# Performance work log

Hardware: AMD Instinct MI355X
Metric: run time of the kernel (lower is better)

Reference implementation:

```python
import jax, jax.numpy as jnp
import numpy as np

GAMMA0 = 1.0


def patch_to_image(patches):
    # patches: [b, n_patch, patch_dim, 1, T] -> image [b, 1, g*p, g*p, T]
    b, n_patch, patch_dim, _, T = patches.shape
    p = int(patch_dim ** 0.5)
    g = int(n_patch ** 0.5)
    img = patches[:, :, :, 0, :]                      # [b, n_patch, p*p, T]
    img = jnp.transpose(img, (0, 3, 1, 2))            # [b, T, n_patch, p*p]
    img = img.reshape(b, T, g, g, p, p)
    img = jnp.transpose(img, (0, 1, 2, 4, 3, 5)).reshape(b, T, 1, g * p, g * p)
    return jnp.transpose(img, (0, 2, 3, 4, 1))        # [b, 1, g*p, g*p, T]


def setup_inputs() -> dict:
    key = jax.random.key(0)
    k0, k1, k2, k3, k4, k5 = jax.random.split(key, 6)
    X = jax.random.normal(k0, (32, 64, 300, 1, 50), dtype=jnp.float32)
    U = jax.random.normal(k1, (32, 1, 40, 1, 50), dtype=jnp.float32)
    x0 = jax.random.normal(k2, (32, 64, 300, 1), dtype=jnp.float32)
    # dictionaries, column-normalized like torch's norm(dim=2, keepdim=True)
    A = jax.random.uniform(k3, (300, 300), dtype=jnp.float32)
    A = A / jnp.linalg.norm(A, axis=0, keepdims=True)
    B = jax.random.uniform(k4, (300, 40), dtype=jnp.float32)
    B = B / jnp.linalg.norm(B, axis=0, keepdims=True)
    C = jax.random.uniform(k5, (256, 300), dtype=jnp.float32)
    C = C / jnp.linalg.norm(C, axis=0, keepdims=True)
    return {"X": X, "U": U, "x0": x0, "A": A, "B": B, "C": C}


def reference(X, U, x0, A, B, C):
    # X: [b, P, 300, 1, T]  U: [b, 1, 40, 1, T]  x0: [b, P, 300, 1]
    # Prediction x_hat_t = A @ x_{t-1}, with x_{-1} = x0 (vectorized over T)
    x_prev = jnp.concatenate([x0[..., None], X[..., :-1]], axis=-1)   # [b,P,300,1,T]
    X_pred = jnp.einsum('ij,bpjut->bpiut', A, x_prev)                 # [b,P,300,1,T]
    # Reconstruction recon_t = C @ x_t, assembled into frames
    recon = jnp.einsum('dj,bpjut->bpdut', C, X)                       # [b,P,256,1,T]
    vid_recon = patch_to_image(recon)                                 # [b,1,128,128,T]
    # Cause state: gamma_t * sum_patches |x_t|
    Bu = jnp.einsum('ij,bqjut->bqiut', B, U)                          # [b,1,300,1,T]
    gamma = GAMMA0 * (1.0 + jnp.exp(-Bu)) / 2.0
    X_U = gamma * jnp.sum(jnp.abs(X), axis=1, keepdims=True)          # [b,1,300,1,T]
    return (vid_recon, X_pred, X_U)
```

## Files before the change

### kernel.cpp

```cpp
#include <hip/hip_runtime.h>

typedef _Float16 half8 __attribute__((ext_vector_type(8)));
typedef _Float16 half4v __attribute__((ext_vector_type(4)));
typedef float f32x4 __attribute__((ext_vector_type(4)));

#define OFF_PRED 26214400
#define OFF_XU   56934400


__global__ void build_M(const float* __restrict__ A, const float* __restrict__ C,
                        _Float16* __restrict__ M) {
    int idx = blockIdx.x * 256 + threadIdx.x;
    if (idx >= 640 * 320) return;
    int e    = idx & 7;
    int lane = (idx >> 3) & 63;
    int fs   = idx >> 9;
    int mt = fs / 10, ks = fs % 10;
    int m = mt * 16 + (lane & 15);
    int k = ks * 32 + (lane >> 4) * 8 + e;
    float v = 0.f;
    if (k < 300) {
        if (m < 256) v = C[m * 300 + k];
        else if (m < 556) v = A[(m - 256) * 300 + k];
    }
    M[idx] = (_Float16)v;
}

__global__ __launch_bounds__(1024, 1) void gemm_main(
    const float* __restrict__ X, const float* __restrict__ x0,
    const _Float16* __restrict__ M, float* __restrict__ out)
{
    __shared__ _Float16 lds[64 * 320];
    char* ldsb = (char*)lds;
    const int bp = blockIdx.x;
    const int b = bp >> 6, p = bp & 63;
    const int tid = threadIdx.x;
    const float* Xbp = X + bp * 15000;

    const int wave = tid >> 6, lane = tid & 63;
    const int lr = lane & 15, lg = lane >> 4;
    const int g = wave >> 1, h = wave & 1;

    if (tid < 320) {
        int row = tid / 5, c = tid % 5;
        *(half4v*)(ldsb + row * 640 + ((600 + c * 8) ^ ((row & 7) << 4))) =
            (half4v){(_Float16)0.f, (_Float16)0.f, (_Float16)0.f, (_Float16)0.f};
    }
    if (tid < 75) {
        const float* s = x0 + bp * 300 + tid * 4;
        half4v h4 = { (_Float16)s[0], (_Float16)s[1], (_Float16)s[2], (_Float16)s[3] };
        *(half4v*)(ldsb + tid * 8) = h4;
    }
    for (int i = tid; i < 3750; i += 1024) {
        int t = i % 50, jq = i / 50;
        const float* s = Xbp + (jq * 4) * 50 + t;
        half4v h4 = { (_Float16)s[0], (_Float16)s[50], (_Float16)s[100], (_Float16)s[150] };
        int row = t + 1;
        *(half4v*)(ldsb + row * 640 + ((jq * 8) ^ ((row & 7) << 4))) = h4;
    }
    __syncthreads();

    f32x4 acc[5][2];
    #pragma unroll
    for (int j = 0; j < 5; j++)
        #pragma unroll
        for (int nt = 0; nt < 2; nt++)
            acc[j][nt] = (f32x4){0.f, 0.f, 0.f, 0.f};

    const _Float16* Mw = M + (g * 5 * 10) * 512 + lane * 8;
    #define LDSA(nt, ks) (*(const half8*)(ldsb + (h * 32 + (nt) * 16 + lr) * 640 + \
                         (((ks) * 64 + lg * 16) ^ ((lr & 7) << 4))))

    #pragma unroll
    for (int ks = 0; ks < 10; ks++) {
        half8 bf0 = *(const half8*)(Mw + (0 * 10 + ks) * 512);
        half8 bf1 = *(const half8*)(Mw + (1 * 10 + ks) * 512);
        half8 bf2 = *(const half8*)(Mw + (2 * 10 + ks) * 512);
        half8 bf3 = *(const half8*)(Mw + (3 * 10 + ks) * 512);
        half8 bf4 = *(const half8*)(Mw + (4 * 10 + ks) * 512);
        #pragma unroll
        for (int nt = 0; nt < 2; nt++) {
            half8 a = LDSA(nt, ks);
            acc[0][nt] = __builtin_amdgcn_mfma_f32_16x16x32_f16(a, bf0, acc[0][nt], 0, 0, 0);
            acc[1][nt] = __builtin_amdgcn_mfma_f32_16x16x32_f16(a, bf1, acc[1][nt], 0, 0, 0);
            acc[2][nt] = __builtin_amdgcn_mfma_f32_16x16x32_f16(a, bf2, acc[2][nt], 0, 0, 0);
            acc[3][nt] = __builtin_amdgcn_mfma_f32_16x16x32_f16(a, bf3, acc[3][nt], 0, 0, 0);
            acc[4][nt] = __builtin_amdgcn_mfma_f32_16x16x32_f16(a, bf4, acc[4][nt], 0, 0, 0);
        }
    }

    const int gr = p >> 3, gc = p & 7;
    #pragma unroll
    for (int j = 0; j < 5; j++) {
        int colm = g * 80 + j * 16 + lr;
        if (colm < 256) {
            int base = b * 819200 + ((gr * 16 + (colm >> 4)) * 128 + gc * 16 + (colm & 15)) * 50;
            #pragma unroll
            for (int nt = 0; nt < 2; nt++) {
                int t0 = h * 32 + nt * 16 + lg * 4;
                if (t0 == 0) {
                    out[base + 0] = acc[j][0][1];
                    out[base + 1] = acc[j][0][2];
                    out[base + 2] = acc[j][0][3];
                } else if (t0 <= 46) {
                    f32x4 v = acc[j][nt];
                    __builtin_memcpy(&out[base + t0 - 1], &v, 16);
                } else if (t0 == 48) {
                    out[base + 47] = acc[j][nt][0];
                    out[base + 48] = acc[j][nt][1];
                    out[base + 49] = acc[j][nt][2];
                }
            }
        } else if (colm < 556) {
            int base = OFF_PRED + (bp * 300 + (colm - 256)) * 50;
            #pragma unroll
            for (int nt = 0; nt < 2; nt++) {
                int t0 = h * 32 + nt * 16 + lg * 4;
                if (t0 <= 46) {
                    f32x4 v = acc[j][nt];
                    __builtin_memcpy(&out[base + t0], &v, 16);
                } else if (t0 == 48) {
                    out[base + 48] = acc[j][nt][0];
                    out[base + 49] = acc[j][nt][1];
                }
            }
        }
    }
}

__global__ void xu_kernel(const float* __restrict__ X, const float* __restrict__ U,
                          const float* __restrict__ B, float* __restrict__ out) {
    int id = blockIdx.x * 256 + threadIdx.x;
    if (id >= 480000) return;
    int t = id % 50;
    int i = (id / 50) % 300;
    int b = id / 15000;
    const float* xp = X + b * 960000 + i * 50 + t;
    float s = 0.f;
    #pragma unroll 8
    for (int pp = 0; pp < 64; pp++) s += fabsf(xp[pp * 15000]);
    float bu = 0.f;
    const float* up = U + b * 2000 + t;
    const float* Bp = B + i * 40;
    #pragma unroll 8
    for (int q = 0; q < 40; q++) bu += Bp[q] * up[q * 50];
    out[OFF_XU + id] = 0.5f * (1.f + expf(-bu)) * s;
}

extern "C" void kernel_launch(void* const* d_in, const int* in_sizes, int n_in,
                              void* d_out, int out_size, void* d_ws, size_t ws_size,
                              hipStream_t stream) {
    const float* X  = (const float*)d_in[0];
    const float* U  = (const float*)d_in[1];
    const float* x0 = (const float*)d_in[2];
    const float* A  = (const float*)d_in[3];
    const float* B  = (const float*)d_in[4];
    const float* C  = (const float*)d_in[5];
    float* out = (float*)d_out;
    _Float16* M = (_Float16*)d_ws;

    build_M<<<800, 256, 0, stream>>>(A, C, M);
    gemm_main<<<2048, 1024, 0, stream>>>(X, x0, M, out);
    xu_kernel<<<1875, 256, 0, stream>>>(X, U, B, out);
}
```

Baseline: 147.1 us.

## Split each patch GEMM block into two half-time blocks for higher occupancy

```diff
diff --git a/kernel.cpp b/kernel.cpp
--- a/kernel.cpp
+++ b/kernel.cpp
@@ -6,7 +6,6 @@
 
 #define OFF_PRED 26214400
 #define OFF_XU   56934400
-
 
 __global__ void build_M(const float* __restrict__ A, const float* __restrict__ C,
                         _Float16* __restrict__ M) {
@@ -26,37 +25,52 @@
     M[idx] = (_Float16)v;
 }
 
-__global__ __launch_bounds__(1024, 1) void gemm_main(
+#define LDSH(r, j, v) *(_Float16*)(ldsb + (r) * 640 + (((j) * 2) ^ (((r) & 7) << 4))) = (v)
+
+__global__ __launch_bounds__(512, 4) void gemm_main(
     const float* __restrict__ X, const float* __restrict__ x0,
     const _Float16* __restrict__ M, float* __restrict__ out)
 {
-    __shared__ _Float16 lds[64 * 320];
+    __shared__ _Float16 lds[32 * 320];
     char* ldsb = (char*)lds;
-    const int bp = blockIdx.x;
+    const int bid = blockIdx.x;
+    const int bp = bid >> 1, h = bid & 1;
     const int b = bp >> 6, p = bp & 63;
     const int tid = threadIdx.x;
     const float* Xbp = X + bp * 15000;
 
     const int wave = tid >> 6, lane = tid & 63;
     const int lr = lane & 15, lg = lane >> 4;
-    const int g = wave >> 1, h = wave & 1;
+    const int g = wave;
 
-    if (tid < 320) {
-        int row = tid / 5, c = tid % 5;
-        *(half4v*)(ldsb + row * 640 + ((600 + c * 8) ^ ((row & 7) << 4))) =
-            (half4v){(_Float16)0.f, (_Float16)0.f, (_Float16)0.f, (_Float16)0.f};
-    }
-    if (tid < 75) {
-        const float* s = x0 + bp * 300 + tid * 4;
-        half4v h4 = { (_Float16)s[0], (_Float16)s[1], (_Float16)s[2], (_Float16)s[3] };
-        *(half4v*)(ldsb + tid * 8) = h4;
-    }
-    for (int i = tid; i < 3750; i += 1024) {
-        int t = i % 50, jq = i / 50;
-        const float* s = Xbp + (jq * 4) * 50 + t;
-        half4v h4 = { (_Float16)s[0], (_Float16)s[50], (_Float16)s[100], (_Float16)s[150] };
-        int row = t + 1;
-        *(half4v*)(ldsb + row * 640 + ((jq * 8) ^ ((row & 7) << 4))) = h4;
+    #pragma unroll
+    for (int it = 0; it < 5; it++)
+        *(unsigned long long*)(ldsb + tid * 8 + it * 4096) = 0ULL;
+    __syncthreads();
+
+    if (h == 0) {
+        if (tid < 75) {
+            f32x4 v = *(const f32x4*)(x0 + bp * 300 + tid * 4);
+            half4v h4 = { (_Float16)v.x, (_Float16)v.y, (_Float16)v.z, (_Float16)v.w };
+            *(half4v*)(ldsb + tid * 8) = h4;
+        }
+        for (int i = tid; i < 4800; i += 512) {
+            int j = i >> 4, pi = i & 15;
+            int t0 = pi * 2;
+            const float* s = Xbp + j * 50 + t0;
+            float v0 = s[0], v1 = s[1];
+            LDSH(t0 + 1, j, (_Float16)v0);
+            if (pi < 15) LDSH(t0 + 2, j, (_Float16)v1);
+        }
+    } else {
+        for (int i = tid; i < 3000; i += 512) {
+            int j = i / 10, pi = i - (i / 10) * 10;
+            int t0 = 30 + pi * 2;
+            const float* s = Xbp + j * 50 + t0;
+            float v0 = s[0], v1 = s[1];
+            if (pi > 0) LDSH(t0 - 31, j, (_Float16)v0);
+            LDSH(t0 - 30, j, (_Float16)v1);
+        }
     }
     __syncthreads();
 
@@ -67,8 +81,8 @@
         for (int nt = 0; nt < 2; nt++)
             acc[j][nt] = (f32x4){0.f, 0.f, 0.f, 0.f};
 
-    const _Float16* Mw = M + (g * 5 * 10) * 512 + lane * 8;
-    #define LDSA(nt, ks) (*(const half8*)(ldsb + (h * 32 + (nt) * 16 + lr) * 640 + \
+    const _Float16* Mw = M + g * 50 * 512 + lane * 8;
+    #define LDSA(nt, ks) (*(const half8*)(ldsb + ((nt) * 16 + lr) * 640 + \
                          (((ks) * 64 + lg * 16) ^ ((lr & 7) << 4))))
 
     #pragma unroll
@@ -160,6 +174,6 @@
     _Float16* M = (_Float16*)d_ws;
 
     build_M<<<800, 256, 0, stream>>>(A, C, M);
-    gemm_main<<<2048, 1024, 0, stream>>>(X, x0, M, out);
+    gemm_main<<<4096, 512, 0, stream>>>(X, x0, M, out);
     xu_kernel<<<1875, 256, 0, stream>>>(X, U, B, out);
 }
```

Result: slower. 179.6 us (+22.1%).

## Make gemm_main persistent over 8 patches with double-buffered LDS prefetch

Applied to the files above, without the earlier changes.

```diff
diff --git a/kernel.cpp b/kernel.cpp
--- a/kernel.cpp
+++ b/kernel.cpp
@@ -6,7 +6,7 @@
 
 #define OFF_PRED 26214400
 #define OFF_XU   56934400
-
+#define NBP 8
 
 __global__ void build_M(const float* __restrict__ A, const float* __restrict__ C,
                         _Float16* __restrict__ M) {
@@ -30,102 +30,157 @@
     const float* __restrict__ X, const float* __restrict__ x0,
     const _Float16* __restrict__ M, float* __restrict__ out)
 {
-    __shared__ _Float16 lds[64 * 320];
-    char* ldsb = (char*)lds;
-    const int bp = blockIdx.x;
-    const int b = bp >> 6, p = bp & 63;
+    extern __shared__ char ldsraw[];
     const int tid = threadIdx.x;
-    const float* Xbp = X + bp * 15000;
-
     const int wave = tid >> 6, lane = tid & 63;
     const int lr = lane & 15, lg = lane >> 4;
     const int g = wave >> 1, h = wave & 1;
-
-    if (tid < 320) {
-        int row = tid / 5, c = tid % 5;
-        *(half4v*)(ldsb + row * 640 + ((600 + c * 8) ^ ((row & 7) << 4))) =
-            (half4v){(_Float16)0.f, (_Float16)0.f, (_Float16)0.f, (_Float16)0.f};
-    }
-    if (tid < 75) {
-        const float* s = x0 + bp * 300 + tid * 4;
-        half4v h4 = { (_Float16)s[0], (_Float16)s[1], (_Float16)s[2], (_Float16)s[3] };
-        *(half4v*)(ldsb + tid * 8) = h4;
-    }
-    for (int i = tid; i < 3750; i += 1024) {
-        int t = i % 50, jq = i / 50;
-        const float* s = Xbp + (jq * 4) * 50 + t;
-        half4v h4 = { (_Float16)s[0], (_Float16)s[50], (_Float16)s[100], (_Float16)s[150] };
-        int row = t + 1;
-        *(half4v*)(ldsb + row * 640 + ((jq * 8) ^ ((row & 7) << 4))) = h4;
-    }
+    const int bp0 = blockIdx.x * NBP;
+
+    int st_t[4], st_j[4];
+    #pragma unroll
+    for (int u = 0; u < 4; u++) { int i = tid + u * 1024; st_t[u] = i % 50; st_j[u] = i / 50; }
+    const bool v3 = tid < 678;
+
+    const _Float16* Mw = M + g * 50 * 512 + lane * 8;
+
+    #pragma unroll
+    for (int u = 0; u < 10; u++)
+        *(unsigned long long*)(ldsraw + tid * 8 + u * 8192) = 0ULL;
     __syncthreads();
 
-    f32x4 acc[5][2];
-    #pragma unroll
-    for (int j = 0; j < 5; j++)
-        #pragma unroll
-        for (int nt = 0; nt < 2; nt++)
-            acc[j][nt] = (f32x4){0.f, 0.f, 0.f, 0.f};
-
-    const _Float16* Mw = M + (g * 5 * 10) * 512 + lane * 8;
-    #define LDSA(nt, ks) (*(const half8*)(ldsb + (h * 32 + (nt) * 16 + lr) * 640 + \
-                         (((ks) * 64 + lg * 16) ^ ((lr & 7) << 4))))
-
-    #pragma unroll
-    for (int ks = 0; ks < 10; ks++) {
-        half8 bf0 = *(const half8*)(Mw + (0 * 10 + ks) * 512);
-        half8 bf1 = *(const half8*)(Mw + (1 * 10 + ks) * 512);
-        half8 bf2 = *(const half8*)(Mw + (2 * 10 + ks) * 512);
-        half8 bf3 = *(const half8*)(Mw + (3 * 10 + ks) * 512);
-        half8 bf4 = *(const half8*)(Mw + (4 * 10 + ks) * 512);
-        #pragma unroll
-        for (int nt = 0; nt < 2; nt++) {
-            half8 a = LDSA(nt, ks);
-            acc[0][nt] = __builtin_amdgcn_mfma_f32_16x16x32_f16(a, bf0, acc[0][nt], 0, 0, 0);
-            acc[1][nt] = __builtin_amdgcn_mfma_f32_16x16x32_f16(a, bf1, acc[1][nt], 0, 0, 0);
-            acc[2][nt] = __builtin_amdgcn_mfma_f32_16x16x32_f16(a, bf2, acc[2][nt], 0, 0, 0);
-            acc[3][nt] = __builtin_amdgcn_mfma_f32_16x16x32_f16(a, bf3, acc[3][nt], 0, 0, 0);
-            acc[4][nt] = __builtin_amdgcn_mfma_f32_16x16x32_f16(a, bf4, acc[4][nt], 0, 0, 0);
-        }
-    }
-
-    const int gr = p >> 3, gc = p & 7;
-    #pragma unroll
-    for (int j = 0; j < 5; j++) {
-        int colm = g * 80 + j * 16 + lr;
-        if (colm < 256) {
-            int base = b * 819200 + ((gr * 16 + (colm >> 4)) * 128 + gc * 16 + (colm & 15)) * 50;
+    float sx[4][4];
+    float s0x[4];
+
+    {
+        const float* Xb = X + bp0 * 15000;
+        #pragma unroll
+        for (int u = 0; u < 4; u++) if (u < 3 || v3) {
+            const float* s = Xb + st_j[u] * 200 + st_t[u];
+            sx[u][0] = s[0]; sx[u][1] = s[50]; sx[u][2] = s[100]; sx[u][3] = s[150];
+        }
+        if (tid < 75) {
+            f32x4 v = *(const f32x4*)(x0 + bp0 * 300 + tid * 4);
+            s0x[0] = v.x; s0x[1] = v.y; s0x[2] = v.z; s0x[3] = v.w;
+        }
+    }
+    {
+        char* wb = ldsraw;
+        #pragma unroll
+        for (int u = 0; u < 4; u++) if (u < 3 || v3) {
+            int row = st_t[u] + 1;
+            half4v h4 = {(_Float16)sx[u][0], (_Float16)sx[u][1], (_Float16)sx[u][2], (_Float16)sx[u][3]};
+            *(half4v*)(wb + row * 640 + ((st_j[u] * 8) ^ ((row & 7) << 4))) = h4;
+        }
+        if (tid < 75) {
+            half4v h4 = {(_Float16)s0x[0], (_Float16)s0x[1], (_Float16)s0x[2], (_Float16)s0x[3]};
+            *(half4v*)(wb + tid * 8) = h4;
+        }
+    }
+    __syncthreads();
+
+    #define LDSA(base, nt, ks) (*(const half8*)((base) + (h * 32 + (nt) * 16 + lr) * 640 + \
+                               (((ks) * 64 + lg * 16) ^ ((lr & 7) << 4))))
+
+    for (int it = 0; it < NBP; ++it) {
+        const int bp = bp0 + it;
+        const int b = bp >> 6, p = bp & 63;
+        char* ldsb = ldsraw + (it & 1) * 40960;
+
+        if (it + 1 < NBP) {
+            const float* Xb = X + (bp + 1) * 15000;
+            #pragma unroll
+            for (int u = 0; u < 4; u++) if (u < 3 || v3) {
+                const float* s = Xb + st_j[u] * 200 + st_t[u];
+                sx[u][0] = s[0]; sx[u][1] = s[50]; sx[u][2] = s[100]; sx[u][3] = s[150];
+            }
+            if (tid < 75) {
+                f32x4 v = *(const f32x4*)(x0 + (bp + 1) * 300 + tid * 4);
+                s0x[0] = v.x; s0x[1] = v.y; s0x[2] = v.z; s0x[3] = v.w;
+            }
+        }
+
+        f32x4 acc[5][2];
+        #pragma unroll
+        for (int j = 0; j < 5; j++)
+            #pragma unroll
+            for (int nt = 0; nt < 2; nt++)
+                acc[j][nt] = (f32x4){0.f, 0.f, 0.f, 0.f};
+
+        #pragma unroll
+        for (int ks = 0; ks < 10; ks++) {
+            half8 bf0 = *(const half8*)(Mw + (0 * 10 + ks) * 512);
+            half8 bf1 = *(const half8*)(Mw + (1 * 10 + ks) * 512);
+            half8 bf2 = *(const half8*)(Mw + (2 * 10 + ks) * 512);
+            half8 bf3 = *(const half8*)(Mw + (3 * 10 + ks) * 512);
+            half8 bf4 = *(const half8*)(Mw + (4 * 10 + ks) * 512);
             #pragma unroll
             for (int nt = 0; nt < 2; nt++) {
-                int t0 = h * 32 + nt * 16 + lg * 4;
-                if (t0 == 0) {
-                    out[base + 0] = acc[j][0][1];
-                    out[base + 1] = acc[j][0][2];
-                    out[base + 2] = acc[j][0][3];
-                } else if (t0 <= 46) {
-                    f32x4 v = acc[j][nt];
-                    __builtin_memcpy(&out[base + t0 - 1], &v, 16);
-                } else if (t0 == 48) {
-                    out[base + 47] = acc[j][nt][0];
-                    out[base + 48] = acc[j][nt][1];
-                    out[base + 49] = acc[j][nt][2];
+                half8 a = LDSA(ldsb, nt, ks);
+                acc[0][nt] = __builtin_amdgcn_mfma_f32_16x16x32_f16(a, bf0, acc[0][nt], 0, 0, 0);
+                acc[1][nt] = __builtin_amdgcn_mfma_f32_16x16x32_f16(a, bf1, acc[1][nt], 0, 0, 0);
+                acc[2][nt] = __builtin_amdgcn_mfma_f32_16x16x32_f16(a, bf2, acc[2][nt], 0, 0, 0);
+                acc[3][nt] = __builtin_amdgcn_mfma_f32_16x16x32_f16(a, bf3, acc[3][nt], 0, 0, 0);
+                acc[4][nt] = __builtin_amdgcn_mfma_f32_16x16x32_f16(a, bf4, acc[4][nt], 0, 0, 0);
+            }
+        }
+
+        {
+            const int gr = p >> 3, gc = p & 7;
+            #pragma unroll
+            for (int j = 0; j < 5; j++) {
+                int colm = g * 80 + j * 16 + lr;
+                if (colm < 256) {
+                    int base = b * 819200 + ((gr * 16 + (colm >> 4)) * 128 + gc * 16 + (colm & 15)) * 50;
+                    #pragma unroll
+                    for (int nt = 0; nt < 2; nt++) {
+                        int t0 = h * 32 + nt * 16 + lg * 4;
+                        if (t0 == 0) {
+                            out[base + 0] = acc[j][0][1];
+                            out[base + 1] = acc[j][0][2];
+                            out[base + 2] = acc[j][0][3];
+                        } else if (t0 <= 46) {
+                            f32x4 v = acc[j][nt];
+                            __builtin_memcpy(&out[base + t0 - 1], &v, 16);
+                        } else if (t0 == 48) {
+                            out[base + 47] = acc[j][nt][0];
+                            out[base + 48] = acc[j][nt][1];
+                            out[base + 49] = acc[j][nt][2];
+                        }
+                    }
+                } else if (colm < 556) {
+                    int base = OFF_PRED + (bp * 300 + (colm - 256)) * 50;
+                    #pragma unroll
+                    for (int nt = 0; nt < 2; nt++) {
+                        int t0 = h * 32 + nt * 16 + lg * 4;
+                        if (t0 <= 46) {
+                            f32x4 v = acc[j][nt];
+                            __builtin_memcpy(&out[base + t0], &v, 16);
+                        } else if (t0 == 48) {
+                            out[base + 48] = acc[j][nt][0];
+                            out[base + 49] = acc[j][nt][1];
+                        }
+                    }
                 }
             }
-        } else if (colm < 556) {
-            int base = OFF_PRED + (bp * 300 + (colm - 256)) * 50;
-            #pragma unroll
-            for (int nt = 0; nt < 2; nt++) {
-                int t0 = h * 32 + nt * 16 + lg * 4;
-                if (t0 <= 46) {
-                    f32x4 v = acc[j][nt];
-                    __builtin_memcpy(&out[base + t0], &v, 16);
-                } else if (t0 == 48) {
-                    out[base + 48] = acc[j][nt][0];
-                    out[base + 49] = acc[j][nt][1];
-                }
-            }
-        }
-    }
+        }
+
+        if (it + 1 < NBP) {
+            char* wb = ldsraw + ((it & 1) ^ 1) * 40960;
+            #pragma unroll
+            for (int u = 0; u < 4; u++) if (u < 3 || v3) {
+                int row = st_t[u] + 1;
+                half4v h4 = {(_Float16)sx[u][0], (_Float16)sx[u][1], (_Float16)sx[u][2], (_Float16)sx[u][3]};
+                *(half4v*)(wb + row * 640 + ((st_j[u] * 8) ^ ((row & 7) << 4))) = h4;
+            }
+            if (tid < 75) {
+                half4v h4 = {(_Float16)s0x[0], (_Float16)s0x[1], (_Float16)s0x[2], (_Float16)s0x[3]};
+                *(half4v*)(wb + tid * 8) = h4;
+            }
+        }
+        __syncthreads();
+    }
+    #undef LDSA
 }
 
 __global__ void xu_kernel(const float* __restrict__ X, const float* __restrict__ U,
@@ -160,6 +215,6 @@
     _Float16* M = (_Float16*)d_ws;
 
     build_M<<<800, 256, 0, stream>>>(A, C, M);
-    gemm_main<<<2048, 1024, 0, stream>>>(X, x0, M, out);
+    gemm_main<<<256, 1024, 81920, stream>>>(X, x0, M, out);
     xu_kernel<<<1875, 256, 0, stream>>>(X, U, B, out);
 }
```

Measured after the change: 541.8 us. +268.4%, slower.
